# Kernel optimization log

Measured on AMD Instinct MI355X. Metric: run time of the kernel, lower is better.

Reference implementation:

```python
import jax, jax.numpy as jnp
import numpy as np

H = 128   # LSTM hidden size
E = 300   # embedding dim
PAD_ID = 0
UNK_ID = 1


def _lstm_dir(x, Wih, Whh, b):
    """Single-direction LSTM. x: [B,S,E] -> hidden states [B,S,H]. PyTorch gate order i,f,g,o."""
    B = x.shape[0]
    def step(carry, xt):
        h, c = carry
        g = xt @ Wih.T + h @ Whh.T + b            # [B,4H]
        i, f, gg, o = jnp.split(g, 4, axis=-1)
        c = jax.nn.sigmoid(f) * c + jax.nn.sigmoid(i) * jnp.tanh(gg)
        h = jax.nn.sigmoid(o) * jnp.tanh(c)
        return (h, c), h
    init = (jnp.zeros((B, H), x.dtype), jnp.zeros((B, H), x.dtype))
    _, hs = jax.lax.scan(step, init, jnp.swapaxes(x, 0, 1))   # [S,B,H]
    return jnp.swapaxes(hs, 0, 1)


def setup_inputs() -> dict:
    key = jax.random.key(0)
    ks = jax.random.split(key, 12)
    B, S, D = 32, 512, 8
    WORD_V, DEP_V, NUM_LABELS = 100000, 64, 5
    inp = {
        "word_ids": jax.random.randint(ks[0], (B, 3, S), 0, WORD_V, dtype=jnp.int32),
        "deps_ids": jax.random.randint(ks[1], (B, S, D), 0, DEP_V, dtype=jnp.int32),
        "word_table": jax.random.normal(ks[2], (WORD_V, E), jnp.float32) * 0.1,
        "dep_table": jax.random.normal(ks[3], (DEP_V, E), jnp.float32) * 0.1,
        "Wih_f": jax.random.normal(ks[4], (4 * H, E), jnp.float32) * 0.05,
        "Whh_f": jax.random.normal(ks[5], (4 * H, H), jnp.float32) * 0.05,
        "b_f": jnp.zeros((4 * H,), jnp.float32),
        "Wih_b": jax.random.normal(ks[6], (4 * H, E), jnp.float32) * 0.05,
        "Whh_b": jax.random.normal(ks[7], (4 * H, H), jnp.float32) * 0.05,
        "b_b": jnp.zeros((4 * H,), jnp.float32),
        "W_cls": jax.random.normal(ks[8], (NUM_LABELS, 2 * H), jnp.float32) * 0.05,
        "b_cls": jnp.zeros((NUM_LABELS,), jnp.float32),
    }
    return inp


def reference(word_ids, deps_ids, word_table, dep_table,
              Wih_f, Whh_f, b_f, Wih_b, Whh_b, b_b, W_cls, b_cls):
    # word_ids[:, 1, :] -> token ids used for word embeddings
    word_embs = word_table[word_ids[:, 1, :]]          # [B,S,E]
    dep_embs = dep_table[deps_ids]                     # [B,S,D,E]

    # vectorized masked mean-pool of dep embeddings (skip pad/unk ids)
    mask = ((deps_ids != PAD_ID) & (deps_ids != UNK_ID)).astype(word_embs.dtype)[..., None]  # [B,S,D,1]
    cnt = mask.sum(axis=2)                             # [B,S,1]
    dep_mean = (dep_embs * mask).sum(axis=2) / jnp.maximum(cnt, 1.0)
    word_embs = jnp.where(cnt > 0, 0.5 * word_embs + 0.5 * dep_mean, word_embs)

    # BiLSTM
    out_f = _lstm_dir(word_embs, Wih_f, Whh_f, b_f)                       # [B,S,H]
    out_b = _lstm_dir(word_embs[:, ::-1, :], Wih_b, Whh_b, b_b)[:, ::-1, :]
    out = jnp.concatenate([out_f, out_b], axis=-1)                        # [B,S,2H]

    # max-pool over time, dropout is identity in eval, then classifier
    pooled = out.max(axis=1)                           # [B,2H]
    logits = pooled @ W_cls.T + b_cls                  # [B,num_labels]
    return logits
```

## Files before the change

kernel.cpp:

```cpp
#include <hip/hip_runtime.h>
#include <hip/hip_bf16.h>
#include <cstdint>
#include <cstddef>

#define S_LEN 512
#define BATCH 32
#define EDIM  300
#define KPAD  320
#define K3    960
#define HDIM  128
#define NGATE 512
#define NCOLS 1024

typedef float    f2  __attribute__((ext_vector_type(2)));
typedef float    f4v __attribute__((ext_vector_type(4)));
typedef short    short8 __attribute__((ext_vector_type(8)));
typedef _Float16 h2  __attribute__((ext_vector_type(2)));

__device__ __forceinline__ float sigm_fast(float x) {
    return __builtin_amdgcn_rcpf(1.f + __expf(-x));
}
__device__ __forceinline__ float tanh_fast(float x) {
    return 2.f * sigm_fast(2.f * x) - 1.f;
}

template <int CTRL>
__device__ __forceinline__ float dpp_mov(float x) {
    int r = __builtin_amdgcn_update_dpp(0, __float_as_int(x), CTRL, 0xF, 0xF, true);
    return __int_as_float(r);
}

__device__ __forceinline__ h2 pk_f16(float a, float b) {
    auto r = __builtin_amdgcn_cvt_pkrtz(a, b);
    return __builtin_bit_cast(h2, r);
}

__device__ __forceinline__ void bf16_split(float v, ushort& hi, ushort& lo) {
    __hip_bfloat16 hb = __float2bfloat16(v);
    float hf = __bfloat162float(hb);
    __hip_bfloat16 lb = __float2bfloat16(v - hf);
    hi = *reinterpret_cast<ushort*>(&hb);
    lo = *reinterpret_cast<ushort*>(&lb);
}

__global__ void embed_xcat(const int* __restrict__ word_ids,
                           const int* __restrict__ deps_ids,
                           const float* __restrict__ word_table,
                           const float* __restrict__ dep_table,
                           ushort* __restrict__ Xcat) {
    int pos = blockIdx.x;
    int b = pos >> 9, s = pos & (S_LEN - 1);
    int wid = word_ids[b * 3 * S_LEN + S_LEN + s];
    const int* dp = deps_ids + (size_t)pos * 8;
    int ids[8];
    int cnt = 0;
#pragma unroll
    for (int d = 0; d < 8; ++d) {
        int id = dp[d];
        ids[d] = id;
        cnt += (id != 0 && id != 1) ? 1 : 0;
    }
    float inv = 0.5f / (float)((cnt > 0) ? cnt : 1);
    const float* wr = word_table + (size_t)wid * EDIM;
    ushort* xr = Xcat + (size_t)pos * K3;
    for (int e = threadIdx.x; e < KPAD; e += 128) {
        float v = 0.f;
        if (e < EDIM) {
            float w = wr[e];
            float dsum = 0.f;
#pragma unroll
            for (int d = 0; d < 8; ++d) {
                if (ids[d] != 0 && ids[d] != 1) dsum += dep_table[ids[d] * EDIM + e];
            }
            v = (cnt > 0) ? (0.5f * w + dsum * inv) : w;
        }
        ushort hu, lu;
        bf16_split(v, hu, lu);
        xr[e] = hu;
        xr[KPAD + e] = hu;
        xr[2 * KPAD + e] = lu;
    }
}

__global__ void wcat_kernel(const float* __restrict__ Wih_f,
                            const float* __restrict__ Wih_b,
                            ushort* __restrict__ Wcat) {
    int n = blockIdx.x;
    const float* src = (n < NGATE) ? (Wih_f + (size_t)n * EDIM)
                                   : (Wih_b + (size_t)(n - NGATE) * EDIM);
    ushort* wr = Wcat + (size_t)n * K3;
    for (int e = threadIdx.x; e < KPAD; e += 128) {
        float v = (e < EDIM) ? src[e] : 0.f;
        ushort hu, lu;
        bf16_split(v, hu, lu);
        wr[e] = hu;
        wr[KPAD + e] = lu;
        wr[2 * KPAD + e] = hu;
    }
}

#define LSTR 40
__global__ __launch_bounds__(256) void gemm_mfma(
        const ushort* __restrict__ Xcat,
        const ushort* __restrict__ Wcat,
        const float* __restrict__ b_f, const float* __restrict__ b_b,
        float* __restrict__ pre) {
    __shared__ ushort Asub[128 * LSTR];
    __shared__ ushort Bsub[128 * LSTR];
    int tid = threadIdx.x;
    int wave = tid >> 6, lane = tid & 63;
    int lid = lane & 15, quad = lane >> 4;
    int m0 = blockIdx.x * 128, n0 = blockIdx.y * 128;
    int wm = (wave >> 1) * 64, wn = (wave & 1) * 64;

    f4v acc[4][4];
#pragma unroll
    for (int i = 0; i < 4; ++i)
#pragma unroll
        for (int j = 0; j < 4; ++j) acc[i][j] = (f4v)0.f;

    float bias[4];
#pragma unroll
    for (int nt = 0; nt < 4; ++nt) {
        int n = n0 + wn + nt * 16 + lid;
        bias[nt] = (n < NGATE) ? b_f[n] : b_b[n - NGATE];
    }

    int c0 = tid, c1 = tid + 256;
    const ushort* aptr0 = Xcat + (size_t)(m0 + (c0 >> 2)) * K3 + (c0 & 3) * 8;
    const ushort* aptr1 = Xcat + (size_t)(m0 + (c1 >> 2)) * K3 + (c1 & 3) * 8;
    const ushort* bptr0 = Wcat + (size_t)(n0 + (c0 >> 2)) * K3 + (c0 & 3) * 8;
    const ushort* bptr1 = Wcat + (size_t)(n0 + (c1 >> 2)) * K3 + (c1 & 3) * 8;
    int la0 = (c0 >> 2) * LSTR + (c0 & 3) * 8;
    int la1 = (c1 >> 2) * LSTR + (c1 & 3) * 8;

    short8 ra0 = *(const short8*)(aptr0);
    short8 ra1 = *(const short8*)(aptr1);
    short8 rb0 = *(const short8*)(bptr0);
    short8 rb1 = *(const short8*)(bptr1);

    for (int k0 = 0; k0 < K3; k0 += 32) {
        __syncthreads();
        *(short8*)&Asub[la0] = ra0;
        *(short8*)&Asub[la1] = ra1;
        *(short8*)&Bsub[la0] = rb0;
        *(short8*)&Bsub[la1] = rb1;
        __syncthreads();
        if (k0 + 32 < K3) {
            ra0 = *(const short8*)(aptr0 + k0 + 32);
            ra1 = *(const short8*)(aptr1 + k0 + 32);
            rb0 = *(const short8*)(bptr0 + k0 + 32);
            rb1 = *(const short8*)(bptr1 + k0 + 32);
        }
        short8 aF[4], bF[4];
#pragma unroll
        for (int mt = 0; mt < 4; ++mt)
            aF[mt] = *(const short8*)&Asub[(wm + mt * 16 + lid) * LSTR + quad * 8];
#pragma unroll
        for (int nt = 0; nt < 4; ++nt)
            bF[nt] = *(const short8*)&Bsub[(wn + nt * 16 + lid) * LSTR + quad * 8];
#pragma unroll
        for (int mt = 0; mt < 4; ++mt)
#pragma unroll
            for (int nt = 0; nt < 4; ++nt)
                acc[mt][nt] = __builtin_amdgcn_mfma_f32_16x16x32_bf16(
                    aF[mt], bF[nt], acc[mt][nt], 0, 0, 0);
    }

#pragma unroll
    for (int mt = 0; mt < 4; ++mt)
#pragma unroll
        for (int nt = 0; nt < 4; ++nt) {
            int n = n0 + wn + nt * 16 + lid;
#pragma unroll
            for (int r = 0; r < 4; ++r) {
                int m = m0 + wm + mt * 16 + quad * 4 + r;
                pre[(size_t)m * NCOLS + n] = acc[mt][nt][r] + bias[nt];
            }
        }
}

__global__ __launch_bounds__(256, 1) void lstm_rec(
        const float* __restrict__ pre,
        const float* __restrict__ Whh_f, const float* __restrict__ Whh_b,
        float* __restrict__ pooled) {
    __shared__ _Float16 h_s[HDIM];
    int t = threadIdx.x;
    int lane = t & 63;
    int wv = t >> 6;
    int tau = lane & 3;
    int ks  = (lane >> 2) & 3;
    int hi2 = lane >> 4;
    int hbase = wv * 32 + hi2 * 8;
    int b = blockIdx.x >> 1;
    int dir = blockIdx.x & 1;
    const float* Whh = dir ? Whh_b : Whh_f;

    h2 w[8][16];
#pragma unroll
    for (int j = 0; j < 8; ++j) {
        const float* rp = Whh + (size_t)(tau * HDIM + hbase + j) * HDIM + ks * 32;
#pragma unroll
        for (int q = 0; q < 16; ++q) w[j][q] = pk_f16(rp[2 * q], rp[2 * q + 1]);
    }

    float c = 0.f;
    float hmax = -1e30f;
    if (t < 64) ((uint*)h_s)[t] = 0u;

    const float* pX = pre + (size_t)b * S_LEN * NCOLS + dir * NGATE
                    + tau * HDIM + hbase + 2 * ks;
    const float* pY = pX + 1;
    int s = dir ? (S_LEN - 1) : 0;
    int sd = dir ? -1 : 1;
    float pXn1 = pX[(long)s * NCOLS], pYn1 = pY[(long)s * NCOLS];
    float pXn2 = pX[(long)(s + sd) * NCOLS], pYn2 = pY[(long)(s + sd) * NCOLS];

    int hZ = hbase + 2 * ks + (tau >> 1);

    asm volatile("s_waitcnt lgkmcnt(0)\n\ts_barrier" ::: "memory");

    for (int step = 0; step < S_LEN; ++step) {
        float curX = pXn1, curY = pYn1;
        pXn1 = pXn2; pYn1 = pYn2;
        if (step + 2 < S_LEN) {
            pXn2 = pX[(long)(s + 2 * sd) * NCOLS];
            pYn2 = pY[(long)(s + 2 * sd) * NCOLS];
        }

        h2 hh[16];
        const h2* hp = (const h2*)h_s;
#pragma unroll
        for (int q = 0; q < 16; ++q) hh[q] = hp[ks * 16 + q];

        float P[8];
#pragma unroll
        for (int j = 0; j < 8; ++j) {
            float acc = 0.f;
#pragma unroll
            for (int q = 0; q < 16; ++q)
                acc = __builtin_amdgcn_fdot2(w[j][q], hh[q], acc, false);
            P[j] = acc;
        }

        float R[8];
#pragma unroll
        for (int j = 0; j < 8; ++j) {
            float r = P[j];
            r += dpp_mov<0x124>(r);
            r += dpp_mov<0x128>(r);
            R[j] = r;
        }

        float X01 = (ks & 1) ? R[2] : R[0];
        float X23 = (ks & 1) ? R[6] : R[4];
        float X   = (ks & 2) ? X23 : X01;
        float Y01 = (ks & 1) ? R[3] : R[1];
        float Y23 = (ks & 1) ? R[7] : R[5];
        float Y   = (ks & 2) ? Y23 : Y01;
        float gX = X + curX;
        float gY = Y + curY;

        float giX = dpp_mov<0x00>(gX), gfX = dpp_mov<0x55>(gX);
        float ggX = dpp_mov<0xAA>(gX), goX = dpp_mov<0xFF>(gX);
        float giY = dpp_mov<0x00>(gY), gfY = dpp_mov<0x55>(gY);
        float ggY = dpp_mov<0xAA>(gY), goY = dpp_mov<0xFF>(gY);

        bool oy = (tau & 2) != 0;
        float gi = oy ? giY : giX;
        float gf = oy ? gfY : gfX;
        float gg = oy ? ggY : ggX;
        float go = oy ? goY : goX;

        c = sigm_fast(gf) * c + sigm_fast(gi) * tanh_fast(gg);
        float h = sigm_fast(go) * tanh_fast(c);
        hmax = fmaxf(hmax, h);

        if ((tau & 1) == 0) h_s[hZ] = (_Float16)h;
        asm volatile("s_waitcnt lgkmcnt(0)\n\ts_barrier" ::: "memory");
        s += sd;
    }

    if ((tau & 1) == 0) pooled[b * 256 + dir * HDIM + hZ] = hmax;
}

__global__ void cls_kernel(const float* __restrict__ pooled,
                           const float* __restrict__ W_cls,
                           const float* __restrict__ b_cls,
                           float* __restrict__ out) {
    int i = threadIdx.x;
    if (i < BATCH * 5) {
        int b = i / 5, l = i % 5;
        float acc = b_cls[l];
        const float* p = pooled + b * 256;
        const float* w = W_cls + l * 256;
#pragma unroll 8
        for (int j = 0; j < 256; ++j) acc = fmaf(p[j], w[j], acc);
        out[i] = acc;
    }
}

extern "C" void kernel_launch(void* const* d_in, const int* in_sizes, int n_in,
                              void* d_out, int out_size, void* d_ws, size_t ws_size,
                              hipStream_t stream) {
    const int*   word_ids   = (const int*)d_in[0];
    const int*   deps_ids   = (const int*)d_in[1];
    const float* word_table = (const float*)d_in[2];
    const float* dep_table  = (const float*)d_in[3];
    const float* Wih_f      = (const float*)d_in[4];
    const float* Whh_f      = (const float*)d_in[5];
    const float* b_f        = (const float*)d_in[6];
    const float* Wih_b      = (const float*)d_in[7];
    const float* Whh_b      = (const float*)d_in[8];
    const float* b_b        = (const float*)d_in[9];
    const float* W_cls      = (const float*)d_in[10];
    const float* b_cls      = (const float*)d_in[11];
    float* out = (float*)d_out;

    float*  pre    = (float*)d_ws;
    float*  pooled = pre + (size_t)BATCH * S_LEN * NCOLS;
    ushort* Xcat   = (ushort*)(pooled + BATCH * 256);
    ushort* Wcat   = Xcat + (size_t)BATCH * S_LEN * K3;

    embed_xcat<<<BATCH * S_LEN, 128, 0, stream>>>(word_ids, deps_ids,
                                                  word_table, dep_table, Xcat);
    wcat_kernel<<<NCOLS, 128, 0, stream>>>(Wih_f, Wih_b, Wcat);
    gemm_mfma<<<dim3(128, 8), 256, 0, stream>>>(Xcat, Wcat, b_f, b_b, pre);
    lstm_rec<<<64, 256, 0, stream>>>(pre, Whh_f, Whh_b, pooled);
    cls_kernel<<<1, 192, 0, stream>>>(pooled, W_cls, b_cls, out);
}
```

Before: 518.1 us.

## Double LSTM recurrence threads to 512 and compute one gate per lane

The recurrent LSTM kernel now uses 512 threads per block instead of 256. Each lane holds half as many Whh rows (4 instead of 8) and produces a single gate pre-activation instead of two. Gate activation is computed once per lane, with sigmoid and tanh sharing one exp, and the activated values are broadcast with DPP instead of the raw pre-activations. The aim is to shorten the serial per-step critical path (fewer dot products per lane, less selection logic), at the cost of more waves taking part in each per-step barrier.

```diff
diff --git a/kernel.cpp b/kernel.cpp
--- a/kernel.cpp
+++ b/kernel.cpp
@@ -180,7 +180,7 @@
         }
 }
 
-__global__ __launch_bounds__(256, 1) void lstm_rec(
+__global__ __launch_bounds__(512, 2) void lstm_rec(
         const float* __restrict__ pre,
         const float* __restrict__ Whh_f, const float* __restrict__ Whh_b,
         float* __restrict__ pooled) {
@@ -191,14 +191,14 @@
     int tau = lane & 3;
     int ks  = (lane >> 2) & 3;
     int hi2 = lane >> 4;
-    int hbase = wv * 32 + hi2 * 8;
+    int hbase = wv * 16 + hi2 * 4;
     int b = blockIdx.x >> 1;
     int dir = blockIdx.x & 1;
     const float* Whh = dir ? Whh_b : Whh_f;
 
-    h2 w[8][16];
-#pragma unroll
-    for (int j = 0; j < 8; ++j) {
+    h2 w[4][16];
+#pragma unroll
+    for (int j = 0; j < 4; ++j) {
         const float* rp = Whh + (size_t)(tau * HDIM + hbase + j) * HDIM + ks * 32;
 #pragma unroll
         for (int q = 0; q < 16; ++q) w[j][q] = pk_f16(rp[2 * q], rp[2 * q + 1]);
@@ -208,34 +208,34 @@
     float hmax = -1e30f;
     if (t < 64) ((uint*)h_s)[t] = 0u;
 
-    const float* pX = pre + (size_t)b * S_LEN * NCOLS + dir * NGATE
-                    + tau * HDIM + hbase + 2 * ks;
-    const float* pY = pX + 1;
-    int s = dir ? (S_LEN - 1) : 0;
+    const float* pZ = pre + (size_t)b * S_LEN * NCOLS + dir * NGATE
+                    + tau * HDIM + hbase + ks;
+    int s0 = dir ? (S_LEN - 1) : 0;
     int sd = dir ? -1 : 1;
-    float pXn1 = pX[(long)s * NCOLS], pYn1 = pY[(long)s * NCOLS];
-    float pXn2 = pX[(long)(s + sd) * NCOLS], pYn2 = pY[(long)(s + sd) * NCOLS];
-
-    int hZ = hbase + 2 * ks + (tau >> 1);
+    long stride = (long)sd * NCOLS;
+    const float* pf = pZ + (long)s0 * NCOLS;
+    float pn1 = *pf; pf += stride;
+    float pn2 = *pf; pf += stride;
+
+    bool is_g = (tau == 2);
+    int hZ = hbase + ks;
+    const h2* hp = (const h2*)h_s + ks * 16;
 
     asm volatile("s_waitcnt lgkmcnt(0)\n\ts_barrier" ::: "memory");
 
     for (int step = 0; step < S_LEN; ++step) {
-        float curX = pXn1, curY = pYn1;
-        pXn1 = pXn2; pYn1 = pYn2;
-        if (step + 2 < S_LEN) {
-            pXn2 = pX[(long)(s + 2 * sd) * NCOLS];
-            pYn2 = pY[(long)(s + 2 * sd) * NCOLS];
-        }
+        float cur = pn1;
+        pn1 = pn2;
+        if (step + 2 < S_LEN) pn2 = *pf;
+        pf += stride;
 
         h2 hh[16];
-        const h2* hp = (const h2*)h_s;
-#pragma unroll
-        for (int q = 0; q < 16; ++q) hh[q] = hp[ks * 16 + q];
-
-        float P[8];
-#pragma unroll
-        for (int j = 0; j < 8; ++j) {
+#pragma unroll
+        for (int q = 0; q < 16; ++q) hh[q] = hp[q];
+
+        float P[4];
+#pragma unroll
+        for (int j = 0; j < 4; ++j) {
             float acc = 0.f;
 #pragma unroll
             for (int q = 0; q < 16; ++q)
@@ -243,45 +243,39 @@
             P[j] = acc;
         }
 
-        float R[8];
-#pragma unroll
-        for (int j = 0; j < 8; ++j) {
+        float R[4];
+#pragma unroll
+        for (int j = 0; j < 4; ++j) {
             float r = P[j];
             r += dpp_mov<0x124>(r);
             r += dpp_mov<0x128>(r);
             R[j] = r;
         }
 
-        float X01 = (ks & 1) ? R[2] : R[0];
-        float X23 = (ks & 1) ? R[6] : R[4];
+        float X01 = (ks & 1) ? R[1] : R[0];
+        float X23 = (ks & 1) ? R[3] : R[2];
         float X   = (ks & 2) ? X23 : X01;
-        float Y01 = (ks & 1) ? R[3] : R[1];
-        float Y23 = (ks & 1) ? R[7] : R[5];
-        float Y   = (ks & 2) ? Y23 : Y01;
-        float gX = X + curX;
-        float gY = Y + curY;
-
-        float giX = dpp_mov<0x00>(gX), gfX = dpp_mov<0x55>(gX);
-        float ggX = dpp_mov<0xAA>(gX), goX = dpp_mov<0xFF>(gX);
-        float giY = dpp_mov<0x00>(gY), gfY = dpp_mov<0x55>(gY);
-        float ggY = dpp_mov<0xAA>(gY), goY = dpp_mov<0xFF>(gY);
-
-        bool oy = (tau & 2) != 0;
-        float gi = oy ? giY : giX;
-        float gf = oy ? gfY : gfX;
-        float gg = oy ? ggY : ggX;
-        float go = oy ? goY : goX;
-
-        c = sigm_fast(gf) * c + sigm_fast(gi) * tanh_fast(gg);
-        float h = sigm_fast(go) * tanh_fast(c);
+        float g   = X + cur;
+
+        float e  = __expf(-g);
+        float sg = __builtin_amdgcn_rcpf(1.f + e);
+        float th = 2.f * __builtin_amdgcn_rcpf(1.f + e * e) - 1.f;
+        float act = is_g ? th : sg;
+
+        float ai = dpp_mov<0x00>(act);
+        float af = dpp_mov<0x55>(act);
+        float ag = dpp_mov<0xAA>(act);
+        float ao = dpp_mov<0xFF>(act);
+
+        c = af * c + ai * ag;
+        float h = ao * tanh_fast(c);
         hmax = fmaxf(hmax, h);
 
-        if ((tau & 1) == 0) h_s[hZ] = (_Float16)h;
+        if (tau == 0) h_s[hZ] = (_Float16)h;
         asm volatile("s_waitcnt lgkmcnt(0)\n\ts_barrier" ::: "memory");
-        s += sd;
-    }
-
-    if ((tau & 1) == 0) pooled[b * 256 + dir * HDIM + hZ] = hmax;
+    }
+
+    if (tau == 0) pooled[b * 256 + dir * HDIM + hZ] = hmax;
 }
 
 __global__ void cls_kernel(const float* __restrict__ pooled,
@@ -326,6 +320,6 @@
                                                   word_table, dep_table, Xcat);
     wcat_kernel<<<NCOLS, 128, 0, stream>>>(Wih_f, Wih_b, Wcat);
     gemm_mfma<<<dim3(128, 8), 256, 0, stream>>>(Xcat, Wcat, b_f, b_b, pre);
-    lstm_rec<<<64, 256, 0, stream>>>(pre, Whh_f, Whh_b, pooled);
+    lstm_rec<<<64, 512, 0, stream>>>(pre, Whh_f, Whh_b, pooled);
     cls_kernel<<<1, 192, 0, stream>>>(pooled, W_cls, b_cls, out);
 }
```

Measured after the change: 541.5 us. +4.5%, slower.
